# Optimization experiments

Hardware: AMD Instinct MI355X
Metric: run time of the kernel (lower is better)

The kernel has to match this reference:

```python
import jax, jax.numpy as jnp
import numpy as np

NUM_HEADS = 8
DIM_HEAD = 32


def setup_inputs() -> dict:
    key = jax.random.key(0)
    k1, k2, k3 = jax.random.split(key, 3)
    dim = 256
    inner = NUM_HEADS * DIM_HEAD  # 256
    x = jax.random.normal(k1, (2, dim, 32, 32, 32), dtype=jnp.float32)
    # Conv1d(kernel_size=1, bias=False) weights == plain matrices [out_ch, in_ch]
    w_qkv = jax.random.normal(k2, (inner * 3, dim), dtype=jnp.float32) * 0.02
    w_out = jax.random.normal(k3, (dim, inner), dtype=jnp.float32) * 0.02
    return {"x": x, "w_qkv": w_qkv, "w_out": w_out}


def reference(x, w_qkv, w_out):
    b, c, h, w, d = x.shape
    n = h * w * d
    x_flat = x.reshape(b, c, n)
    # 1x1 conv == channel matmul: [b, 3*inner, n]
    qkv = jnp.einsum('oc,bcn->bon', w_qkv, x_flat)
    q, k, v = jnp.split(qkv, 3, axis=1)

    def to_heads(t):  # [b, inner, n] -> [b, H, n, Dh]
        return t.reshape(b, NUM_HEADS, DIM_HEAD, n).transpose(0, 1, 3, 2)

    q = jax.nn.softmax(to_heads(q), axis=-1)   # softmax over dim_head
    k = jax.nn.softmax(to_heads(k), axis=-2)   # softmax over tokens n
    v = to_heads(v)
    # context: [b, H, Dh, Dh]
    context = jnp.einsum('bhnd,bhne->bhde', k, v)
    attn_out = jnp.einsum('bhnd,bhde->bhne', q, context)  # [b, H, n, Dh]
    attn_out = attn_out.transpose(0, 1, 3, 2).reshape(b, NUM_HEADS * DIM_HEAD, n)
    out = jnp.einsum('oi,bin->bon', w_out, attn_out)  # to_out 1x1 conv (dropout=0)
    return out.reshape(b, c, h, w, d)
```

## Files before the change

kernel.cpp:

```cpp
#include <hip/hip_runtime.h>

#define NTOK 32768

typedef __attribute__((ext_vector_type(8))) short  bf16x8;
typedef __attribute__((ext_vector_type(8))) unsigned short u16x8;
typedef __attribute__((ext_vector_type(4))) float  f32x4;

__device__ __forceinline__ unsigned short f32_to_bf16(float f) {
    unsigned int u = __float_as_uint(f);
    u += 0x7FFFu + ((u >> 16) & 1u);
    return (unsigned short)(u >> 16);
}
__device__ __forceinline__ float bf16_to_f32(unsigned short h) {
    return __uint_as_float(((unsigned int)h) << 16);
}

template <typename BT, typename CT, bool QSOFT>
__global__ __launch_bounds__(256) void gemm_mfma(
    const unsigned short* __restrict__ A, const BT* __restrict__ B,
    CT* __restrict__ C, long sA, long sB, long sC)
{
    const int bz = blockIdx.z;
    A += (long)bz * sA; B += (long)bz * sB; C += (long)bz * sC;
    const int row0 = blockIdx.x * 128;
    const int col0 = blockIdx.y * 128;

    __shared__ unsigned short As[128 * 40];

    const int t = threadIdx.x;
    const int wn = t >> 6, lane = t & 63;
    const int m16 = lane & 15, quad = lane >> 4;

    const int sr = t >> 2;
    const int sseg = t & 3;

    f32x4 acc[8][2] = {};

    for (int kk = 0; kk < 8; ++kk) {
        const int k0 = kk * 32;

        __syncthreads();

        bf16x8 a_ld[2];
        #pragma unroll
        for (int h = 0; h < 2; ++h)
            a_ld[h] = *(const bf16x8*)&A[(size_t)(row0 + sr + h * 64) * 256 + k0 + sseg * 8];

        bf16x8 bf[2];
        const BT* bp = B + (size_t)(k0 + quad * 8) * NTOK + col0 + wn * 32 + m16;
        #pragma unroll
        for (int nt = 0; nt < 2; ++nt) {
            const BT* bpn = bp + nt * 16;
            #pragma unroll
            for (int j = 0; j < 8; ++j) {
                BT v = bpn[(size_t)j * NTOK];
                if constexpr (sizeof(BT) == 4)
                    bf[nt][j] = (short)f32_to_bf16((float)v);
                else
                    bf[nt][j] = (short)(unsigned short)v;
            }
        }

        #pragma unroll
        for (int h = 0; h < 2; ++h)
            *(bf16x8*)&As[(sr + h * 64) * 40 + sseg * 8] = a_ld[h];
        __syncthreads();

        #pragma unroll
        for (int mt = 0; mt < 8; ++mt) {
            const bf16x8 af = *(const bf16x8*)&As[(mt * 16 + m16) * 40 + quad * 8];
            #pragma unroll
            for (int nt = 0; nt < 2; ++nt)
                acc[mt][nt] = __builtin_amdgcn_mfma_f32_16x16x32_bf16(
                    af, bf[nt], acc[mt][nt], 0, 0, 0);
        }
    }

    if (QSOFT && row0 < 256) {
        #pragma unroll
        for (int hj = 0; hj < 4; ++hj) {
            #pragma unroll
            for (int nt = 0; nt < 2; ++nt) {
                float mx = -1e30f;
                #pragma unroll
                for (int p = 0; p < 2; ++p)
                    #pragma unroll
                    for (int r = 0; r < 4; ++r)
                        mx = fmaxf(mx, acc[hj * 2 + p][nt][r]);
                mx = fmaxf(mx, __shfl_xor(mx, 16, 64));
                mx = fmaxf(mx, __shfl_xor(mx, 32, 64));
                float s = 0.f;
                #pragma unroll
                for (int p = 0; p < 2; ++p)
                    #pragma unroll
                    for (int r = 0; r < 4; ++r) {
                        const float e = __expf(acc[hj * 2 + p][nt][r] - mx);
                        acc[hj * 2 + p][nt][r] = e;
                        s += e;
                    }
                s += __shfl_xor(s, 16, 64);
                s += __shfl_xor(s, 32, 64);
                const float inv = 1.0f / s;
                #pragma unroll
                for (int p = 0; p < 2; ++p)
                    #pragma unroll
                    for (int r = 0; r < 4; ++r)
                        acc[hj * 2 + p][nt][r] *= inv;
            }
        }
    }

    #pragma unroll
    for (int mt = 0; mt < 8; ++mt) {
        #pragma unroll
        for (int nt = 0; nt < 2; ++nt) {
            #pragma unroll
            for (int r = 0; r < 4; ++r) {
                const int row = row0 + mt * 16 + quad * 4 + r;
                const int col = col0 + wn * 32 + nt * 16 + m16;
                if constexpr (sizeof(CT) == 4)
                    C[(size_t)row * NTOK + col] = acc[mt][nt][r];
                else
                    C[(size_t)row * NTOK + col] = f32_to_bf16(acc[mt][nt][r]);
            }
        }
    }
}

__global__ __launch_bounds__(256) void cast_bf16_kernel(
    const float* __restrict__ src, unsigned short* __restrict__ dst, int n4)
{
    const int i = blockIdx.x * 256 + threadIdx.x;
    if (i < n4) {
        float4 v = ((const float4*)src)[i];
        ushort4 o;
        o.x = f32_to_bf16(v.x); o.y = f32_to_bf16(v.y);
        o.z = f32_to_bf16(v.z); o.w = f32_to_bf16(v.w);
        ((ushort4*)dst)[i] = o;
    }
}

#define CTILE 128
__global__ __launch_bounds__(256) void ctx_kernel(
    const unsigned short* __restrict__ qkv,
    float* __restrict__ num, float* __restrict__ den, int tokens_per_block)
{
    const int chunk = blockIdx.x, h = blockIdx.y, b = blockIdx.z;
    const int n0 = chunk * tokens_per_block;
    const unsigned short* kbase = qkv + ((long)b * 768 + 256 + h * 32) * NTOK;
    const unsigned short* vbase = qkv + ((long)b * 768 + 512 + h * 32) * NTOK;

    __shared__ float ks[32][CTILE + 2];
    __shared__ float vs[32][CTILE + 2];

    const int t = threadIdx.x;
    const int d = t >> 3, eg = t & 7;
    const int lrow = t >> 3, lf = t & 7;

    float acc[4] = {0.f, 0.f, 0.f, 0.f};
    float dsum = 0.f;

    for (int tile = 0; tile < tokens_per_block; tile += CTILE) {
        #pragma unroll
        for (int j = 0; j < 2; ++j) {
            const int f = lf * 2 + j;
            const long g = (long)lrow * NTOK + n0 + tile + f * 8;
            u16x8 kv = *(const u16x8*)&kbase[g];
            u16x8 vv = *(const u16x8*)&vbase[g];
            #pragma unroll
            for (int e = 0; e < 8; ++e) {
                ks[lrow][f * 8 + e] = __expf(bf16_to_f32(kv[e]));
                vs[lrow][f * 8 + e] = bf16_to_f32(vv[e]);
            }
        }
        __syncthreads();
        for (int tok = 0; tok < CTILE; ++tok) {
            const float ek = ks[d][tok];
            dsum += ek;
            #pragma unroll
            for (int i = 0; i < 4; ++i) acc[i] += ek * vs[eg * 4 + i][tok];
        }
        __syncthreads();
    }
    float* nrow = num + (((long)(b * 8 + h) * 32 + d) * 32);
    #pragma unroll
    for (int i = 0; i < 4; ++i) atomicAdd(&nrow[eg * 4 + i], acc[i]);
    if (eg == 0) atomicAdd(&den[b * 256 + h * 32 + d], dsum);
}

__global__ __launch_bounds__(256) void combine_kernel(
    const float* __restrict__ w_out, const float* __restrict__ num,
    const float* __restrict__ den, unsigned short* __restrict__ W2)
{
    const int tid = blockIdx.x * 256 + threadIdx.x;
    const int b = tid >> 16;
    const int rem = tid & 65535;
    const int o = rem >> 8;
    const int i = rem & 255;
    const int h = i >> 5, d = i & 31;
    const float* wrow = w_out + o * 256 + h * 32;
    const float* nrow = num + (((long)(b * 8 + h) * 32 + d) << 5);
    float s = 0.f;
    #pragma unroll
    for (int e = 0; e < 32; ++e) s += wrow[e] * nrow[e];
    W2[tid] = f32_to_bf16(s / den[b * 256 + h * 32 + d]);
}

extern "C" void kernel_launch(void* const* d_in, const int* in_sizes, int n_in,
                              void* d_out, int out_size, void* d_ws, size_t ws_size,
                              hipStream_t stream)
{
    const float* x     = (const float*)d_in[0];
    const float* w_qkv = (const float*)d_in[1];
    const float* w_out = (const float*)d_in[2];
    float* out = (float*)d_out;

    unsigned short* qkv_bf = (unsigned short*)d_ws;
    const long qkv_elems = 2L * 768 * NTOK;
    unsigned short* wqkv_bf = qkv_bf + qkv_elems;
    unsigned short* W2 = wqkv_bf + 768 * 256;
    float* num  = (float*)(W2 + 2 * 256 * 256);
    float* den  = num + 16384;

    hipMemsetAsync(num, 0, (16384 + 512) * sizeof(float), stream);

    cast_bf16_kernel<<<192, 256, 0, stream>>>(w_qkv, wqkv_bf, 768 * 256 / 4);

    gemm_mfma<float, unsigned short, true><<<dim3(6, 256, 2), 256, 0, stream>>>(
        wqkv_bf, x, qkv_bf, 0L, 256L * NTOK, 768L * NTOK);

    ctx_kernel<<<dim3(16, 8, 2), 256, 0, stream>>>(qkv_bf, num, den, NTOK / 16);

    combine_kernel<<<512, 256, 0, stream>>>(w_out, num, den, W2);

    gemm_mfma<unsigned short, float, false><<<dim3(2, 256, 2), 256, 0, stream>>>(
        W2, qkv_bf, out, 65536L, 768L * NTOK, 256L * NTOK);
}
```

Measured before the change: 276.6 us.

## Keep B tile stationary in LDS and loop over M chunks in GEMMs

```diff
diff --git a/kernel.cpp b/kernel.cpp
--- a/kernel.cpp
+++ b/kernel.cpp
@@ -15,113 +15,115 @@
     return __uint_as_float(((unsigned int)h) << 16);
 }
 
-template <typename BT, typename CT, bool QSOFT>
-__global__ __launch_bounds__(256) void gemm_mfma(
+template <typename BT, typename CT, int MCHUNKS, bool QSOFT>
+__global__ __launch_bounds__(256) void gemm_bstat(
     const unsigned short* __restrict__ A, const BT* __restrict__ B,
     CT* __restrict__ C, long sA, long sB, long sC)
 {
-    const int bz = blockIdx.z;
+    const int bz = blockIdx.y;
     A += (long)bz * sA; B += (long)bz * sB; C += (long)bz * sC;
-    const int row0 = blockIdx.x * 128;
-    const int col0 = blockIdx.y * 128;
-
-    __shared__ unsigned short As[128 * 40];
+    const int col0 = blockIdx.x * 128;
+
+    __shared__ unsigned short Bs[128 * 256];
 
     const int t = threadIdx.x;
-    const int wn = t >> 6, lane = t & 63;
+    const int wave = t >> 6, lane = t & 63;
+    const int wm = wave >> 1, wn = wave & 1;
     const int m16 = lane & 15, quad = lane >> 4;
 
-    const int sr = t >> 2;
-    const int sseg = t & 3;
-
-    f32x4 acc[8][2] = {};
-
-    for (int kk = 0; kk < 8; ++kk) {
-        const int k0 = kk * 32;
-
-        __syncthreads();
-
-        bf16x8 a_ld[2];
+    {
+        const int n = t & 127;
+        const int kg0 = (t >> 7) * 16;
+        const int key = n & 7;
+        const BT* bcol = B + col0 + n;
         #pragma unroll
-        for (int h = 0; h < 2; ++h)
-            a_ld[h] = *(const bf16x8*)&A[(size_t)(row0 + sr + h * 64) * 256 + k0 + sseg * 8];
-
-        bf16x8 bf[2];
-        const BT* bp = B + (size_t)(k0 + quad * 8) * NTOK + col0 + wn * 32 + m16;
+        for (int g = 0; g < 16; ++g) {
+            const int kg = kg0 + g;
+            unsigned short tmp[8];
+            #pragma unroll
+            for (int i = 0; i < 8; ++i) {
+                BT v = bcol[(size_t)(kg * 8 + i) * NTOK];
+                if constexpr (sizeof(BT) == 4) tmp[i] = f32_to_bf16((float)v);
+                else                           tmp[i] = (unsigned short)v;
+            }
+            *(u16x8*)&Bs[n * 256 + ((kg ^ key) * 8)] = *(const u16x8*)tmp;
+        }
+    }
+    __syncthreads();
+
+    const int swk = m16 & 7;
+
+    for (int mc = 0; mc < MCHUNKS; ++mc) {
+        const int m0 = mc * 128;
+        f32x4 acc[4][4] = {};
+
+        const unsigned short* Abase = A + (size_t)(m0 + wm * 64 + m16) * 256 + quad * 8;
+
         #pragma unroll
-        for (int nt = 0; nt < 2; ++nt) {
-            const BT* bpn = bp + nt * 16;
-            #pragma unroll
-            for (int j = 0; j < 8; ++j) {
-                BT v = bpn[(size_t)j * NTOK];
-                if constexpr (sizeof(BT) == 4)
-                    bf[nt][j] = (short)f32_to_bf16((float)v);
-                else
-                    bf[nt][j] = (short)(unsigned short)v;
+        for (int kk = 0; kk < 8; ++kk) {
+            bf16x8 bf[4];
+            #pragma unroll
+            for (int nt = 0; nt < 4; ++nt) {
+                const int col = wn * 64 + nt * 16 + m16;
+                bf[nt] = *(const bf16x8*)&Bs[col * 256 + (((kk * 4 + quad) ^ swk) * 8)];
+            }
+            #pragma unroll
+            for (int mt = 0; mt < 4; ++mt) {
+                const bf16x8 af = *(const bf16x8*)&Abase[(size_t)mt * 16 * 256 + kk * 32];
+                #pragma unroll
+                for (int nt = 0; nt < 4; ++nt)
+                    acc[mt][nt] = __builtin_amdgcn_mfma_f32_16x16x32_bf16(
+                        af, bf[nt], acc[mt][nt], 0, 0, 0);
+            }
+        }
+
+        if (QSOFT && m0 < 256) {
+            #pragma unroll
+            for (int hj = 0; hj < 2; ++hj) {
+                #pragma unroll
+                for (int nt = 0; nt < 4; ++nt) {
+                    float mx = -1e30f;
+                    #pragma unroll
+                    for (int p = 0; p < 2; ++p)
+                        #pragma unroll
+                        for (int r = 0; r < 4; ++r)
+                            mx = fmaxf(mx, acc[hj * 2 + p][nt][r]);
+                    mx = fmaxf(mx, __shfl_xor(mx, 16, 64));
+                    mx = fmaxf(mx, __shfl_xor(mx, 32, 64));
+                    float s = 0.f;
+                    #pragma unroll
+                    for (int p = 0; p < 2; ++p)
+                        #pragma unroll
+                        for (int r = 0; r < 4; ++r) {
+                            const float e = __expf(acc[hj * 2 + p][nt][r] - mx);
+                            acc[hj * 2 + p][nt][r] = e;
+                            s += e;
+                        }
+                    s += __shfl_xor(s, 16, 64);
+                    s += __shfl_xor(s, 32, 64);
+                    const float inv = 1.0f / s;
+                    #pragma unroll
+                    for (int p = 0; p < 2; ++p)
+                        #pragma unroll
+                        for (int r = 0; r < 4; ++r)
+                            acc[hj * 2 + p][nt][r] *= inv;
+                }
             }
         }
 
         #pragma unroll
-        for (int h = 0; h < 2; ++h)
-            *(bf16x8*)&As[(sr + h * 64) * 40 + sseg * 8] = a_ld[h];
-        __syncthreads();
-
-        #pragma unroll
-        for (int mt = 0; mt < 8; ++mt) {
-            const bf16x8 af = *(const bf16x8*)&As[(mt * 16 + m16) * 40 + quad * 8];
-            #pragma unroll
-            for (int nt = 0; nt < 2; ++nt)
-                acc[mt][nt] = __builtin_amdgcn_mfma_f32_16x16x32_bf16(
-                    af, bf[nt], acc[mt][nt], 0, 0, 0);
-        }
-    }
-
-    if (QSOFT && row0 < 256) {
-        #pragma unroll
-        for (int hj = 0; hj < 4; ++hj) {
-            #pragma unroll
-            for (int nt = 0; nt < 2; ++nt) {
-                float mx = -1e30f;
+        for (int mt = 0; mt < 4; ++mt) {
+            #pragma unroll
+            for (int nt = 0; nt < 4; ++nt) {
                 #pragma unroll
-                for (int p = 0; p < 2; ++p)
-                    #pragma unroll
-                    for (int r = 0; r < 4; ++r)
-                        mx = fmaxf(mx, acc[hj * 2 + p][nt][r]);
-                mx = fmaxf(mx, __shfl_xor(mx, 16, 64));
-                mx = fmaxf(mx, __shfl_xor(mx, 32, 64));
-                float s = 0.f;
-                #pragma unroll
-                for (int p = 0; p < 2; ++p)
-                    #pragma unroll
-                    for (int r = 0; r < 4; ++r) {
-                        const float e = __expf(acc[hj * 2 + p][nt][r] - mx);
-                        acc[hj * 2 + p][nt][r] = e;
-                        s += e;
-                    }
-                s += __shfl_xor(s, 16, 64);
-                s += __shfl_xor(s, 32, 64);
-                const float inv = 1.0f / s;
-                #pragma unroll
-                for (int p = 0; p < 2; ++p)
-                    #pragma unroll
-                    for (int r = 0; r < 4; ++r)
-                        acc[hj * 2 + p][nt][r] *= inv;
-            }
-        }
-    }
-
-    #pragma unroll
-    for (int mt = 0; mt < 8; ++mt) {
-        #pragma unroll
-        for (int nt = 0; nt < 2; ++nt) {
-            #pragma unroll
-            for (int r = 0; r < 4; ++r) {
-                const int row = row0 + mt * 16 + quad * 4 + r;
-                const int col = col0 + wn * 32 + nt * 16 + m16;
-                if constexpr (sizeof(CT) == 4)
-                    C[(size_t)row * NTOK + col] = acc[mt][nt][r];
-                else
-                    C[(size_t)row * NTOK + col] = f32_to_bf16(acc[mt][nt][r]);
+                for (int r = 0; r < 4; ++r) {
+                    const int row = m0 + wm * 64 + mt * 16 + quad * 4 + r;
+                    const int col = col0 + wn * 64 + nt * 16 + m16;
+                    if constexpr (sizeof(CT) == 4)
+                        C[(size_t)row * NTOK + col] = acc[mt][nt][r];
+                    else
+                        C[(size_t)row * NTOK + col] = f32_to_bf16(acc[mt][nt][r]);
+                }
             }
         }
     }
@@ -151,7 +153,7 @@
     const unsigned short* vbase = qkv + ((long)b * 768 + 512 + h * 32) * NTOK;
 
     __shared__ float ks[32][CTILE + 2];
-    __shared__ float vs[32][CTILE + 2];
+    __shared__ float vs[CTILE][36];
 
     const int t = threadIdx.x;
     const int d = t >> 3, eg = t & 7;
@@ -161,24 +163,20 @@
     float dsum = 0.f;
 
     for (int tile = 0; tile < tokens_per_block; tile += CTILE) {
-        #pragma unroll
-        for (int j = 0; j < 2; ++j) {
-            const int f = lf * 2 + j;
-            const long g = (long)lrow * NTOK + n0 + tile + f * 8;
-            u16x8 kv = *(const u16x8*)&kbase[g];
-            u16x8 vv = *(const u16x8*)&vbase[g];
-            #pragma unroll
-            for (int e = 0; e < 8; ++e) {
-                ks[lrow][f * 8 + e] = __expf(bf16_to_f32(kv[e]));
-                vs[lrow][f * 8 + e] = bf16_to_f32(vv[e]);
-            }
+        #pragma unroll 4
+        for (int jj = 0; jj < 16; ++jj) {
+            const int tok = lf + 8 * jj;
+            const long g = (long)lrow * NTOK + n0 + tile + tok;
+            ks[lrow][tok] = __expf(bf16_to_f32(kbase[g]));
+            vs[tok][lrow] = bf16_to_f32(vbase[g]);
         }
         __syncthreads();
         for (int tok = 0; tok < CTILE; ++tok) {
             const float ek = ks[d][tok];
             dsum += ek;
-            #pragma unroll
-            for (int i = 0; i < 4; ++i) acc[i] += ek * vs[eg * 4 + i][tok];
+            const float4 vv = *(const float4*)&vs[tok][eg * 4];
+            acc[0] += ek * vv.x; acc[1] += ek * vv.y;
+            acc[2] += ek * vv.z; acc[3] += ek * vv.w;
         }
         __syncthreads();
     }
@@ -226,13 +224,13 @@
 
     cast_bf16_kernel<<<192, 256, 0, stream>>>(w_qkv, wqkv_bf, 768 * 256 / 4);
 
-    gemm_mfma<float, unsigned short, true><<<dim3(6, 256, 2), 256, 0, stream>>>(
+    gemm_bstat<float, unsigned short, 6, true><<<dim3(256, 2), 256, 0, stream>>>(
         wqkv_bf, x, qkv_bf, 0L, 256L * NTOK, 768L * NTOK);
 
-    ctx_kernel<<<dim3(16, 8, 2), 256, 0, stream>>>(qkv_bf, num, den, NTOK / 16);
+    ctx_kernel<<<dim3(32, 8, 2), 256, 0, stream>>>(qkv_bf, num, den, NTOK / 32);
 
     combine_kernel<<<512, 256, 0, stream>>>(w_out, num, den, W2);
 
-    gemm_mfma<unsigned short, float, false><<<dim3(2, 256, 2), 256, 0, stream>>>(
+    gemm_bstat<unsigned short, float, 2, false><<<dim3(256, 2), 256, 0, stream>>>(
         W2, qkv_bf, out, 65536L, 768L * NTOK, 256L * NTOK);
 }
```

Measured after the change: 271.6 us. Within noise of the previous version (-1.8%).
